# Performance work log

Measured on AMD Instinct MI355X. Metric: run time of the kernel, lower is better.

Reference implementation:

```python
import jax, jax.numpy as jnp
import numpy as np

N = 8192  # number of nodes


def _deg_norm(idx, n):
    # degree^{-1/2}, zero-degree clamped to 1 (DGL allow_zero_in_degree behavior)
    deg = jax.ops.segment_sum(jnp.ones(idx.shape[0], jnp.float32), idx, num_segments=n)
    return jax.lax.rsqrt(jnp.maximum(deg, 1.0))


def _graph_conv(h, src, dst, norm_src, norm_dst, W, b):
    # norm='both': scale at src, sparse sum-aggregate, scale at dst, then linear
    h = h * norm_src[:, None]
    m = jax.ops.segment_sum(h[src], dst, num_segments=h.shape[0])  # gather + scatter-add
    m = m * norm_dst[:, None]
    return m @ W + b


def setup_inputs() -> dict:
    key = jax.random.key(0)
    k = jax.random.split(key, 6)
    E = 262144
    x = jax.random.normal(k[0], (N, 256), jnp.float32)
    src = jax.random.randint(k[1], (E,), 0, N, jnp.int32)
    dst = jax.random.randint(k[2], (E,), 0, N, jnp.int32)
    W1 = jax.random.normal(k[3], (256, 128), jnp.float32) * (1.0 / np.sqrt(256))
    b1 = jnp.zeros((128,), jnp.float32)
    W2 = jax.random.normal(k[4], (128, 128), jnp.float32) * (1.0 / np.sqrt(128))
    b2 = jnp.zeros((128,), jnp.float32)
    return {"x": x, "src": src, "dst": dst, "W1": W1, "b1": b1, "W2": W2, "b2": b2}


def reference(x, src, dst, W1, b1, W2, b2):
    n = x.shape[0]
    norm_src = _deg_norm(src, n)  # out-degree norm
    norm_dst = _deg_norm(dst, n)  # in-degree norm
    # encode: GraphConv -> relu -> GraphConv  (dropout=0 -> identity)
    h = jax.nn.relu(_graph_conv(x, src, dst, norm_src, norm_dst, W1, b1))
    h = _graph_conv(h, src, dst, norm_src, norm_dst, W2, b2)
    # decode: sigmoid(h h^T), dense [N, N] reconstruction
    return jax.nn.sigmoid(h @ h.T)
```

## Files before the change

kernel.cpp:

```cpp
#include <hip/hip_runtime.h>
#include <hip/hip_bf16.h>

typedef __attribute__((ext_vector_type(8))) short short8;
typedef __attribute__((ext_vector_type(4))) float f32x4;

#define NNODES 8192
#define FDIM 128

__global__ void k_zero(int* __restrict__ p, int n) {
    int i = blockIdx.x * blockDim.x + threadIdx.x;
    if (i < n) p[i] = 0;
}

__global__ void k_deg_int(const int* __restrict__ src, const int* __restrict__ dst,
                          int* __restrict__ cnt_s, int* __restrict__ cnt_d, int E) {
    int e = blockIdx.x * blockDim.x + threadIdx.x;
    if (e < E) {
        atomicAdd(&cnt_s[src[e]], 1);
        atomicAdd(&cnt_d[dst[e]], 1);
    }
}

__global__ __launch_bounds__(256) void k_scan_norms(const int* __restrict__ cnt_s,
                                                    const int* __restrict__ cnt_d,
                                                    float* __restrict__ norm_s,
                                                    int* __restrict__ row_start,
                                                    int* __restrict__ cursor, int n) {
    __shared__ int partial[256];
    __shared__ int offs[257];
    int t = threadIdx.x;
    int base = t * 32;
#pragma unroll
    for (int i = 0; i < 32; ++i)
        norm_s[base + i] = rsqrtf(fmaxf((float)cnt_s[base + i], 1.0f));
    int local[32];
    int s = 0;
#pragma unroll
    for (int i = 0; i < 32; ++i) { local[i] = s; s += cnt_d[base + i]; }
    partial[t] = s;
    __syncthreads();
    if (t == 0) {
        int acc = 0;
        for (int i = 0; i < 256; ++i) { offs[i] = acc; acc += partial[i]; }
        offs[256] = acc;
    }
    __syncthreads();
    int o = offs[t];
#pragma unroll
    for (int i = 0; i < 32; ++i) {
        int v = o + local[i];
        row_start[base + i] = v;
        cursor[base + i] = v;
    }
    if (t == 0) row_start[n] = offs[256];
}

__global__ void k_fill(const int* __restrict__ src, const int* __restrict__ dst,
                       int* __restrict__ cursor, int* __restrict__ csr_src, int E) {
    int e = blockIdx.x * blockDim.x + threadIdx.x;
    if (e < E) {
        int pos = atomicAdd(&cursor[dst[e]], 1);
        csr_src[pos] = src[e];
    }
}

template<int K>
__global__ __launch_bounds__(256) void k_linear(const float* __restrict__ X,
                                                const float* __restrict__ W,
                                                const float* __restrict__ norm,
                                                float* __restrict__ Y) {
    __shared__ float xs[16][K];
    int t = threadIdx.x;
    int row0 = blockIdx.x * 16;
    constexpr int K4 = K / 4;
    constexpr int NCH = 16 * K4 / 256;
#pragma unroll
    for (int i = 0; i < NCH; ++i) {
        int c = t + i * 256;
        int r = c / K4, k4 = c % K4;
        *(float4*)&xs[r][k4 * 4] = *(const float4*)(X + (size_t)(row0 + r) * K + k4 * 4);
    }
    __syncthreads();

    int lane = t & 31, g = t >> 5;
    int r0 = g * 2, r1 = g * 2 + 1;
    int c = lane * 4;
    f32x4 acc0 = {0.f, 0.f, 0.f, 0.f}, acc1 = {0.f, 0.f, 0.f, 0.f};
    for (int k = 0; k < K; k += 4) {
        f32x4 x0 = *(f32x4*)&xs[r0][k];
        f32x4 x1 = *(f32x4*)&xs[r1][k];
#pragma unroll
        for (int kk = 0; kk < 4; ++kk) {
            f32x4 w = *(const f32x4*)(W + (size_t)(k + kk) * FDIM + c);
            acc0 += w * x0[kk];
            acc1 += w * x1[kk];
        }
    }
    float n0 = norm[row0 + r0], n1 = norm[row0 + r1];
    *(f32x4*)(Y + (size_t)(row0 + r0) * FDIM + c) = acc0 * n0;
    *(f32x4*)(Y + (size_t)(row0 + r1) * FDIM + c) = acc1 * n1;
}

static __device__ inline unsigned short f2bf(float f) {
    union { float f; unsigned int u; } a; a.f = f;
    unsigned int u = a.u;
    unsigned int r = u + 0x7FFFu + ((u >> 16) & 1u);
    return (unsigned short)(r >> 16);
}

template<int MODE>
__global__ __launch_bounds__(256) void k_gather_agg(const float* __restrict__ Y,
                                                    const int* __restrict__ row_start,
                                                    const int* __restrict__ csr_src,
                                                    const float* __restrict__ bias,
                                                    void* __restrict__ outp) {
    int t = threadIdx.x;
    int node = blockIdx.x * 8 + (t >> 5);
    int c4 = (t & 31) << 2;
    int beg = row_start[node], end = row_start[node + 1];
    f32x4 acc0 = {0.f, 0.f, 0.f, 0.f}, acc1 = {0.f, 0.f, 0.f, 0.f};
    int e = beg;
    for (; e + 3 < end; e += 4) {
        int s0 = csr_src[e], s1 = csr_src[e + 1], s2 = csr_src[e + 2], s3 = csr_src[e + 3];
        f32x4 v0 = *(const f32x4*)(Y + ((size_t)s0 << 7) + c4);
        f32x4 v1 = *(const f32x4*)(Y + ((size_t)s1 << 7) + c4);
        f32x4 v2 = *(const f32x4*)(Y + ((size_t)s2 << 7) + c4);
        f32x4 v3 = *(const f32x4*)(Y + ((size_t)s3 << 7) + c4);
        acc0 += v0; acc1 += v1; acc0 += v2; acc1 += v3;
    }
    for (; e < end; ++e) {
        int s0 = csr_src[e];
        acc0 += *(const f32x4*)(Y + ((size_t)s0 << 7) + c4);
    }
    f32x4 acc = acc0 + acc1;
    float scale = rsqrtf(fmaxf((float)(end - beg), 1.0f));
    f32x4 b = *(const f32x4*)(bias + c4);
    f32x4 v = acc * scale + b;
    if (MODE == 0) {
#pragma unroll
        for (int i = 0; i < 4; ++i) v[i] = fmaxf(v[i], 0.f);
        *(f32x4*)((float*)outp + ((size_t)node << 7) + c4) = v;
    } else {
        ushort4 u;
        u.x = f2bf(v[0]); u.y = f2bf(v[1]); u.z = f2bf(v[2]); u.w = f2bf(v[3]);
        *(ushort4*)((unsigned short*)outp + ((size_t)node << 7) + c4) = u;
    }
}

__global__ __launch_bounds__(256) void k_decode(const __hip_bfloat16* __restrict__ H,
                                                float* __restrict__ C) {
    const int ti = blockIdx.x, tj = blockIdx.y;
    if (tj < ti) return;
    __shared__ __align__(16) unsigned char smem[65536];
    unsigned char* sA = smem;
    unsigned char* sB = smem + 32768;
    const int t = threadIdx.x;
    const unsigned char* gH = (const unsigned char*)H;

#pragma unroll
    for (int i = 0; i < 8; ++i) {
        int chunk = t + i * 256;
        int row = chunk >> 4;
        int cc = (chunk & 15) << 4;
        int lofs = row * 256 + (cc ^ ((row & 7) << 4));
        *(float4*)(sA + lofs) = *(const float4*)(gH + ((size_t)(ti * 128 + row) << 8) + cc);
        *(float4*)(sB + lofs) = *(const float4*)(gH + ((size_t)(tj * 128 + row) << 8) + cc);
    }
    __syncthreads();

    const int w = t >> 6, lane = t & 63;
    const int wr = (w >> 1) * 64, wc = (w & 1) * 64;
    const int lr = lane & 15;
    const int lk = (lane >> 4) * 16;

    f32x4 acc[4][4] = {};

#pragma unroll
    for (int ks = 0; ks < 4; ++ks) {
        short8 af[4], bfr[4];
#pragma unroll
        for (int mi = 0; mi < 4; ++mi) {
            int row = wr + mi * 16 + lr;
            int off = row * 256 + ((ks * 64 + lk) ^ ((row & 7) << 4));
            af[mi] = *(const short8*)(sA + off);
        }
#pragma unroll
        for (int ni = 0; ni < 4; ++ni) {
            int row = wc + ni * 16 + lr;
            int off = row * 256 + ((ks * 64 + lk) ^ ((row & 7) << 4));
            bfr[ni] = *(const short8*)(sB + off);
        }
#pragma unroll
        for (int mi = 0; mi < 4; ++mi)
#pragma unroll
            for (int ni = 0; ni < 4; ++ni)
                acc[mi][ni] = __builtin_amdgcn_mfma_f32_16x16x32_bf16(af[mi], bfr[ni],
                                                                      acc[mi][ni], 0, 0, 0);
    }

    const int rbase = (lane >> 4) * 4;
    const int cbase = lane & 15;
#pragma unroll
    for (int mi = 0; mi < 4; ++mi) {
        int rowb = ti * 128 + wr + mi * 16 + rbase;
#pragma unroll
        for (int ni = 0; ni < 4; ++ni) {
            int col = tj * 128 + wc + ni * 16 + cbase;
            f32x4 s;
#pragma unroll
            for (int r = 0; r < 4; ++r)
                s[r] = 1.0f / (1.0f + __expf(-acc[mi][ni][r]));
            __builtin_nontemporal_store(s, (f32x4*)(C + (size_t)col * NNODES + rowb));
            if (ti != tj) {
#pragma unroll
                for (int r = 0; r < 4; ++r)
                    __builtin_nontemporal_store(s[r], C + (size_t)(rowb + r) * NNODES + col);
            }
        }
    }
}

extern "C" void kernel_launch(void* const* d_in, const int* in_sizes, int n_in,
                              void* d_out, int out_size, void* d_ws, size_t ws_size,
                              hipStream_t stream) {
    const float* x  = (const float*)d_in[0];
    const int* src  = (const int*)d_in[1];
    const int* dst  = (const int*)d_in[2];
    const float* W1 = (const float*)d_in[3];
    const float* b1 = (const float*)d_in[4];
    const float* W2 = (const float*)d_in[5];
    const float* b2 = (const float*)d_in[6];
    float* out = (float*)d_out;
    const int E = in_sizes[1];

    char* ws = (char*)d_ws;
    float* norm_s    = (float*)(ws + 0);
    int*   cnt_s     = (int*)(ws + (64 << 10));
    int*   cnt_d     = (int*)(ws + (96 << 10));
    int*   row_start = (int*)(ws + (128 << 10));
    int*   cursor    = (int*)(ws + (164 << 10));
    int*   csr_src   = (int*)(ws + (196 << 10));
    char*  big       = ws + (196 << 10) + ((size_t)E * 4);
    float* bufA      = (float*)big;
    float* bufB      = (float*)(big + (4 << 20));
    __hip_bfloat16* h2bf = (__hip_bfloat16*)(big + (8 << 20));

    k_zero<<<(2 * NNODES + 255) / 256, 256, 0, stream>>>(cnt_s, 2 * NNODES);

    k_deg_int<<<(E + 255) / 256, 256, 0, stream>>>(src, dst, cnt_s, cnt_d, E);
    k_scan_norms<<<1, 256, 0, stream>>>(cnt_s, cnt_d, norm_s, row_start, cursor, NNODES);
    k_fill<<<(E + 255) / 256, 256, 0, stream>>>(src, dst, cursor, csr_src, E);

    k_linear<256><<<NNODES / 16, 256, 0, stream>>>(x, W1, norm_s, bufA);
    k_gather_agg<0><<<NNODES / 8, 256, 0, stream>>>(bufA, row_start, csr_src, b1, bufB);

    k_linear<128><<<NNODES / 16, 256, 0, stream>>>(bufB, W2, norm_s, bufA);
    k_gather_agg<1><<<NNODES / 8, 256, 0, stream>>>(bufA, row_start, csr_src, b2, h2bf);

    k_decode<<<dim3(64, 64), 256, 0, stream>>>(h2bf, out);
}
```

Baseline: 211.9 us.

## Fuse encoder into cooperative persistent kernel and drop decode symmetry trick

Merges the degree count, scan, CSR fill, two linear layers and two gathers into one cooperative kernel with grid-wide syncs, keeping multi-kernel launches only as a fallback. This removes per-kernel launch gaps in the encoder but restricts it to 256 blocks. The decode kernel now computes every tile of the full N×N output instead of only the upper triangle with mirrored writes, and uses a fast reciprocal with plain row-major stores. That doubles the MFMA work in exchange for fully coalesced stores in place of strided transposed ones.

```diff
diff --git a/kernel.cpp b/kernel.cpp
--- a/kernel.cpp
+++ b/kernel.cpp
@@ -1,11 +1,168 @@
 #include <hip/hip_runtime.h>
 #include <hip/hip_bf16.h>
+#include <hip/hip_cooperative_groups.h>
+
+namespace cg = cooperative_groups;
 
 typedef __attribute__((ext_vector_type(8))) short short8;
 typedef __attribute__((ext_vector_type(4))) float f32x4;
 
 #define NNODES 8192
 #define FDIM 128
+
+static __device__ inline unsigned short f2bf(float f) {
+    union { float f; unsigned int u; } a; a.f = f;
+    unsigned int u = a.u;
+    unsigned int r = u + 0x7FFFu + ((u >> 16) & 1u);
+    return (unsigned short)(r >> 16);
+}
+
+template<int K>
+__device__ void lin_phase(const float* __restrict__ X, const float* __restrict__ W,
+                          const float* __restrict__ norm, float* __restrict__ Y,
+                          float* xs) {
+    const int t = threadIdx.x;
+    constexpr int K4 = K / 4;
+    constexpr int NCH = 16 * K4 / 256;
+    for (int tile = blockIdx.x; tile < NNODES / 16; tile += gridDim.x) {
+        int row0 = tile * 16;
+        __syncthreads();
+#pragma unroll
+        for (int i = 0; i < NCH; ++i) {
+            int c = t + i * 256;
+            int r = c / K4, k4 = c % K4;
+            *(float4*)&xs[r * K + k4 * 4] = *(const float4*)(X + (size_t)(row0 + r) * K + k4 * 4);
+        }
+        __syncthreads();
+        int lane = t & 31, g = t >> 5;
+        int r0 = g * 2, r1 = r0 + 1;
+        int c = lane * 4;
+        f32x4 acc0 = {0.f, 0.f, 0.f, 0.f}, acc1 = {0.f, 0.f, 0.f, 0.f};
+        for (int k = 0; k < K; k += 4) {
+            f32x4 x0 = *(f32x4*)&xs[r0 * K + k];
+            f32x4 x1 = *(f32x4*)&xs[r1 * K + k];
+#pragma unroll
+            for (int kk = 0; kk < 4; ++kk) {
+                f32x4 w = *(const f32x4*)(W + (size_t)(k + kk) * FDIM + c);
+                acc0 += w * x0[kk];
+                acc1 += w * x1[kk];
+            }
+        }
+        float n0 = norm[row0 + r0], n1 = norm[row0 + r1];
+        *(f32x4*)(Y + (size_t)(row0 + r0) * FDIM + c) = acc0 * n0;
+        *(f32x4*)(Y + (size_t)(row0 + r1) * FDIM + c) = acc1 * n1;
+    }
+}
+
+template<int MODE>
+__device__ void gather_phase(const float* __restrict__ Y, const int* __restrict__ row_start,
+                             const int* __restrict__ csr_src, const float* __restrict__ bias,
+                             void* __restrict__ outp) {
+    const int t = threadIdx.x;
+    const int c4 = (t & 31) << 2;
+    for (int node0 = blockIdx.x * 8; node0 < NNODES; node0 += gridDim.x * 8) {
+        int node = node0 + (t >> 5);
+        int beg = row_start[node], end = row_start[node + 1];
+        f32x4 acc0 = {0.f, 0.f, 0.f, 0.f}, acc1 = {0.f, 0.f, 0.f, 0.f};
+        int e = beg;
+        for (; e + 3 < end; e += 4) {
+            int s0 = csr_src[e], s1 = csr_src[e + 1], s2 = csr_src[e + 2], s3 = csr_src[e + 3];
+            f32x4 v0 = *(const f32x4*)(Y + ((size_t)s0 << 7) + c4);
+            f32x4 v1 = *(const f32x4*)(Y + ((size_t)s1 << 7) + c4);
+            f32x4 v2 = *(const f32x4*)(Y + ((size_t)s2 << 7) + c4);
+            f32x4 v3 = *(const f32x4*)(Y + ((size_t)s3 << 7) + c4);
+            acc0 += v0; acc1 += v1; acc0 += v2; acc1 += v3;
+        }
+        for (; e < end; ++e) {
+            int s0 = csr_src[e];
+            acc0 += *(const f32x4*)(Y + ((size_t)s0 << 7) + c4);
+        }
+        f32x4 acc = acc0 + acc1;
+        float scale = rsqrtf(fmaxf((float)(end - beg), 1.0f));
+        f32x4 b = *(const f32x4*)(bias + c4);
+        f32x4 v = acc * scale + b;
+        if (MODE == 0) {
+#pragma unroll
+            for (int i = 0; i < 4; ++i) v[i] = fmaxf(v[i], 0.f);
+            *(f32x4*)((float*)outp + ((size_t)node << 7) + c4) = v;
+        } else {
+            ushort4 u;
+            u.x = f2bf(v[0]); u.y = f2bf(v[1]); u.z = f2bf(v[2]); u.w = f2bf(v[3]);
+            *(ushort4*)((unsigned short*)outp + ((size_t)node << 7) + c4) = u;
+        }
+    }
+}
+
+struct EncArgs {
+    const int* src; const int* dst; int E;
+    int* cnt;
+    float* norm_s; int* row_start; int* cursor; int* csr_src;
+    const float* x; const float* W1; const float* b1;
+    const float* W2; const float* b2;
+    float* bufA; float* bufB; unsigned short* h2;
+};
+
+__global__ __launch_bounds__(256) void k_encode(EncArgs a) {
+    cg::grid_group grid = cg::this_grid();
+    __shared__ __align__(16) float xs[16 * 256];
+    const int t = threadIdx.x;
+    const int gid = blockIdx.x * 256 + t;
+    const int gsz = gridDim.x * 256;
+
+    for (int i = gid; i < 2 * NNODES; i += gsz) a.cnt[i] = 0;
+    grid.sync();
+
+    for (int e = gid; e < a.E; e += gsz) {
+        atomicAdd(&a.cnt[a.src[e]], 1);
+        atomicAdd(&a.cnt[NNODES + a.dst[e]], 1);
+    }
+    grid.sync();
+
+    for (int i = gid; i < NNODES; i += gsz)
+        a.norm_s[i] = rsqrtf(fmaxf((float)a.cnt[i], 1.0f));
+    if (blockIdx.x == 0) {
+        int* partial = (int*)xs;
+        int* offs = partial + 256;
+        const int* cnt_d = a.cnt + NNODES;
+        int base = t * 32;
+        int local[32];
+        int s = 0;
+#pragma unroll
+        for (int i = 0; i < 32; ++i) { local[i] = s; s += cnt_d[base + i]; }
+        partial[t] = s;
+        __syncthreads();
+        if (t == 0) {
+            int acc = 0;
+            for (int i = 0; i < 256; ++i) { offs[i] = acc; acc += partial[i]; }
+            offs[256] = acc;
+        }
+        __syncthreads();
+        int o = offs[t];
+#pragma unroll
+        for (int i = 0; i < 32; ++i) {
+            int v = o + local[i];
+            a.row_start[base + i] = v;
+            a.cursor[base + i] = v;
+        }
+        if (t == 0) a.row_start[NNODES] = offs[256];
+    }
+    grid.sync();
+
+    for (int e = gid; e < a.E; e += gsz) {
+        int pos = atomicAdd(&a.cursor[a.dst[e]], 1);
+        a.csr_src[pos] = a.src[e];
+    }
+    lin_phase<256>(a.x, a.W1, a.norm_s, a.bufA, xs);
+    grid.sync();
+
+    gather_phase<0>(a.bufA, a.row_start, a.csr_src, a.b1, a.bufB);
+    grid.sync();
+
+    lin_phase<128>(a.bufB, a.W2, a.norm_s, a.bufA, xs);
+    grid.sync();
+
+    gather_phase<1>(a.bufA, a.row_start, a.csr_src, a.b2, a.h2);
+}
 
 __global__ void k_zero(int* __restrict__ p, int n) {
     int i = blockIdx.x * blockDim.x + threadIdx.x;
@@ -13,16 +170,15 @@
 }
 
 __global__ void k_deg_int(const int* __restrict__ src, const int* __restrict__ dst,
-                          int* __restrict__ cnt_s, int* __restrict__ cnt_d, int E) {
+                          int* __restrict__ cnt, int E) {
     int e = blockIdx.x * blockDim.x + threadIdx.x;
     if (e < E) {
-        atomicAdd(&cnt_s[src[e]], 1);
-        atomicAdd(&cnt_d[dst[e]], 1);
-    }
-}
-
-__global__ __launch_bounds__(256) void k_scan_norms(const int* __restrict__ cnt_s,
-                                                    const int* __restrict__ cnt_d,
+        atomicAdd(&cnt[src[e]], 1);
+        atomicAdd(&cnt[NNODES + dst[e]], 1);
+    }
+}
+
+__global__ __launch_bounds__(256) void k_scan_norms(const int* __restrict__ cnt,
                                                     float* __restrict__ norm_s,
                                                     int* __restrict__ row_start,
                                                     int* __restrict__ cursor, int n) {
@@ -30,9 +186,10 @@
     __shared__ int offs[257];
     int t = threadIdx.x;
     int base = t * 32;
+    const int* cnt_d = cnt + NNODES;
 #pragma unroll
     for (int i = 0; i < 32; ++i)
-        norm_s[base + i] = rsqrtf(fmaxf((float)cnt_s[base + i], 1.0f));
+        norm_s[base + i] = rsqrtf(fmaxf((float)cnt[base + i], 1.0f));
     int local[32];
     int s = 0;
 #pragma unroll
@@ -65,95 +222,29 @@
 }
 
 template<int K>
-__global__ __launch_bounds__(256) void k_linear(const float* __restrict__ X,
-                                                const float* __restrict__ W,
-                                                const float* __restrict__ norm,
-                                                float* __restrict__ Y) {
-    __shared__ float xs[16][K];
-    int t = threadIdx.x;
-    int row0 = blockIdx.x * 16;
-    constexpr int K4 = K / 4;
-    constexpr int NCH = 16 * K4 / 256;
-#pragma unroll
-    for (int i = 0; i < NCH; ++i) {
-        int c = t + i * 256;
-        int r = c / K4, k4 = c % K4;
-        *(float4*)&xs[r][k4 * 4] = *(const float4*)(X + (size_t)(row0 + r) * K + k4 * 4);
-    }
-    __syncthreads();
-
-    int lane = t & 31, g = t >> 5;
-    int r0 = g * 2, r1 = g * 2 + 1;
-    int c = lane * 4;
-    f32x4 acc0 = {0.f, 0.f, 0.f, 0.f}, acc1 = {0.f, 0.f, 0.f, 0.f};
-    for (int k = 0; k < K; k += 4) {
-        f32x4 x0 = *(f32x4*)&xs[r0][k];
-        f32x4 x1 = *(f32x4*)&xs[r1][k];
-#pragma unroll
-        for (int kk = 0; kk < 4; ++kk) {
-            f32x4 w = *(const f32x4*)(W + (size_t)(k + kk) * FDIM + c);
-            acc0 += w * x0[kk];
-            acc1 += w * x1[kk];
-        }
-    }
-    float n0 = norm[row0 + r0], n1 = norm[row0 + r1];
-    *(f32x4*)(Y + (size_t)(row0 + r0) * FDIM + c) = acc0 * n0;
-    *(f32x4*)(Y + (size_t)(row0 + r1) * FDIM + c) = acc1 * n1;
-}
-
-static __device__ inline unsigned short f2bf(float f) {
-    union { float f; unsigned int u; } a; a.f = f;
-    unsigned int u = a.u;
-    unsigned int r = u + 0x7FFFu + ((u >> 16) & 1u);
-    return (unsigned short)(r >> 16);
+__global__ __launch_bounds__(256) void k_lin(const float* __restrict__ X,
+                                             const float* __restrict__ W,
+                                             const float* __restrict__ norm,
+                                             float* __restrict__ Y) {
+    __shared__ __align__(16) float xs[16 * K];
+    lin_phase<K>(X, W, norm, Y, xs);
 }
 
 template<int MODE>
-__global__ __launch_bounds__(256) void k_gather_agg(const float* __restrict__ Y,
-                                                    const int* __restrict__ row_start,
-                                                    const int* __restrict__ csr_src,
-                                                    const float* __restrict__ bias,
-                                                    void* __restrict__ outp) {
-    int t = threadIdx.x;
-    int node = blockIdx.x * 8 + (t >> 5);
-    int c4 = (t & 31) << 2;
-    int beg = row_start[node], end = row_start[node + 1];
-    f32x4 acc0 = {0.f, 0.f, 0.f, 0.f}, acc1 = {0.f, 0.f, 0.f, 0.f};
-    int e = beg;
-    for (; e + 3 < end; e += 4) {
-        int s0 = csr_src[e], s1 = csr_src[e + 1], s2 = csr_src[e + 2], s3 = csr_src[e + 3];
-        f32x4 v0 = *(const f32x4*)(Y + ((size_t)s0 << 7) + c4);
-        f32x4 v1 = *(const f32x4*)(Y + ((size_t)s1 << 7) + c4);
-        f32x4 v2 = *(const f32x4*)(Y + ((size_t)s2 << 7) + c4);
-        f32x4 v3 = *(const f32x4*)(Y + ((size_t)s3 << 7) + c4);
-        acc0 += v0; acc1 += v1; acc0 += v2; acc1 += v3;
-    }
-    for (; e < end; ++e) {
-        int s0 = csr_src[e];
-        acc0 += *(const f32x4*)(Y + ((size_t)s0 << 7) + c4);
-    }
-    f32x4 acc = acc0 + acc1;
-    float scale = rsqrtf(fmaxf((float)(end - beg), 1.0f));
-    f32x4 b = *(const f32x4*)(bias + c4);
-    f32x4 v = acc * scale + b;
-    if (MODE == 0) {
-#pragma unroll
-        for (int i = 0; i < 4; ++i) v[i] = fmaxf(v[i], 0.f);
-        *(f32x4*)((float*)outp + ((size_t)node << 7) + c4) = v;
-    } else {
-        ushort4 u;
-        u.x = f2bf(v[0]); u.y = f2bf(v[1]); u.z = f2bf(v[2]); u.w = f2bf(v[3]);
-        *(ushort4*)((unsigned short*)outp + ((size_t)node << 7) + c4) = u;
-    }
+__global__ __launch_bounds__(256) void k_gat(const float* __restrict__ Y,
+                                             const int* __restrict__ row_start,
+                                             const int* __restrict__ csr_src,
+                                             const float* __restrict__ bias,
+                                             void* __restrict__ outp) {
+    gather_phase<MODE>(Y, row_start, csr_src, bias, outp);
 }
 
 __global__ __launch_bounds__(256) void k_decode(const __hip_bfloat16* __restrict__ H,
                                                 float* __restrict__ C) {
-    const int ti = blockIdx.x, tj = blockIdx.y;
-    if (tj < ti) return;
     __shared__ __align__(16) unsigned char smem[65536];
     unsigned char* sA = smem;
     unsigned char* sB = smem + 32768;
+    const int ti = blockIdx.x, tj = blockIdx.y;
     const int t = threadIdx.x;
     const unsigned char* gH = (const unsigned char*)H;
 
@@ -206,15 +297,10 @@
 #pragma unroll
         for (int ni = 0; ni < 4; ++ni) {
             int col = tj * 128 + wc + ni * 16 + cbase;
-            f32x4 s;
-#pragma unroll
-            for (int r = 0; r < 4; ++r)
-                s[r] = 1.0f / (1.0f + __expf(-acc[mi][ni][r]));
-            __builtin_nontemporal_store(s, (f32x4*)(C + (size_t)col * NNODES + rowb));
-            if (ti != tj) {
-#pragma unroll
-                for (int r = 0; r < 4; ++r)
-                    __builtin_nontemporal_store(s[r], C + (size_t)(rowb + r) * NNODES + col);
+#pragma unroll
+            for (int r = 0; r < 4; ++r) {
+                float s = __builtin_amdgcn_rcpf(1.0f + __expf(-acc[mi][ni][r]));
+                C[(size_t)(rowb + r) * NNODES + col] = s;
             }
         }
     }
@@ -235,27 +321,36 @@
 
     char* ws = (char*)d_ws;
     float* norm_s    = (float*)(ws + 0);
-    int*   cnt_s     = (int*)(ws + (64 << 10));
-    int*   cnt_d     = (int*)(ws + (96 << 10));
-    int*   row_start = (int*)(ws + (128 << 10));
-    int*   cursor    = (int*)(ws + (164 << 10));
-    int*   csr_src   = (int*)(ws + (196 << 10));
-    char*  big       = ws + (196 << 10) + ((size_t)E * 4);
+    int*   cnt       = (int*)(ws + (32 << 10));
+    int*   row_start = (int*)(ws + (96 << 10));
+    int*   cursor    = (int*)(ws + (132 << 10));
+    int*   csr_src   = (int*)(ws + (164 << 10));
+    char*  big       = ws + (164 << 10) + ((size_t)E * 4);
     float* bufA      = (float*)big;
     float* bufB      = (float*)(big + (4 << 20));
     __hip_bfloat16* h2bf = (__hip_bfloat16*)(big + (8 << 20));
 
-    k_zero<<<(2 * NNODES + 255) / 256, 256, 0, stream>>>(cnt_s, 2 * NNODES);
-
-    k_deg_int<<<(E + 255) / 256, 256, 0, stream>>>(src, dst, cnt_s, cnt_d, E);
-    k_scan_norms<<<1, 256, 0, stream>>>(cnt_s, cnt_d, norm_s, row_start, cursor, NNODES);
-    k_fill<<<(E + 255) / 256, 256, 0, stream>>>(src, dst, cursor, csr_src, E);
-
-    k_linear<256><<<NNODES / 16, 256, 0, stream>>>(x, W1, norm_s, bufA);
-    k_gather_agg<0><<<NNODES / 8, 256, 0, stream>>>(bufA, row_start, csr_src, b1, bufB);
-
-    k_linear<128><<<NNODES / 16, 256, 0, stream>>>(bufB, W2, norm_s, bufA);
-    k_gather_agg<1><<<NNODES / 8, 256, 0, stream>>>(bufA, row_start, csr_src, b2, h2bf);
+    EncArgs ea;
+    ea.src = src; ea.dst = dst; ea.E = E;
+    ea.cnt = cnt; ea.norm_s = norm_s; ea.row_start = row_start;
+    ea.cursor = cursor; ea.csr_src = csr_src;
+    ea.x = x; ea.W1 = W1; ea.b1 = b1; ea.W2 = W2; ea.b2 = b2;
+    ea.bufA = bufA; ea.bufB = bufB; ea.h2 = (unsigned short*)h2bf;
+
+    void* kp[] = { &ea };
+    hipError_t cerr = hipLaunchCooperativeKernel((const void*)k_encode, dim3(256), dim3(256),
+                                                 kp, 0, stream);
+    if (cerr != hipSuccess) {
+        (void)hipGetLastError();
+        k_zero<<<(2 * NNODES + 255) / 256, 256, 0, stream>>>(cnt, 2 * NNODES);
+        k_deg_int<<<(E + 255) / 256, 256, 0, stream>>>(src, dst, cnt, E);
+        k_scan_norms<<<1, 256, 0, stream>>>(cnt, norm_s, row_start, cursor, NNODES);
+        k_fill<<<(E + 255) / 256, 256, 0, stream>>>(src, dst, cursor, csr_src, E);
+        k_lin<256><<<NNODES / 16, 256, 0, stream>>>(x, W1, norm_s, bufA);
+        k_gat<0><<<NNODES / 8, 256, 0, stream>>>(bufA, row_start, csr_src, b1, bufB);
+        k_lin<128><<<NNODES / 16, 256, 0, stream>>>(bufB, W2, norm_s, bufA);
+        k_gat<1><<<NNODES / 8, 256, 0, stream>>>(bufA, row_start, csr_src, b2, h2bf);
+    }
 
     k_decode<<<dim3(64, 64), 256, 0, stream>>>(h2bf, out);
 }
```

Result: slower. 392.0 us (+85.0%).

## Fuse second linear into first aggregation and compute full decode grid

Applied to the files above, without the earlier changes.

The first gather-aggregate now runs the W2 projection itself from shared memory, which removes one kernel launch and an 8192x128 intermediate round trip. The decoder no longer exploits symmetry: every block computes its own tile and writes it row-major with normal stores, where before only upper-triangle tiles ran and each wrote both the tile and its transpose. This doubles the MFMA work in exchange for coalesced, non-transposed writes. It also merges the degree counters into one array, shrinks the zeroing launch and uses a hardware reciprocal for the sigmoid.

```diff
diff --git a/kernel.cpp b/kernel.cpp
--- a/kernel.cpp
+++ b/kernel.cpp
@@ -6,6 +6,13 @@
 
 #define NNODES 8192
 #define FDIM 128
+
+static __device__ inline unsigned short f2bf(float f) {
+    union { float f; unsigned int u; } a; a.f = f;
+    unsigned int u = a.u;
+    unsigned int r = u + 0x7FFFu + ((u >> 16) & 1u);
+    return (unsigned short)(r >> 16);
+}
 
 __global__ void k_zero(int* __restrict__ p, int n) {
     int i = blockIdx.x * blockDim.x + threadIdx.x;
@@ -13,16 +20,15 @@
 }
 
 __global__ void k_deg_int(const int* __restrict__ src, const int* __restrict__ dst,
-                          int* __restrict__ cnt_s, int* __restrict__ cnt_d, int E) {
+                          int* __restrict__ cnt, int E) {
     int e = blockIdx.x * blockDim.x + threadIdx.x;
     if (e < E) {
-        atomicAdd(&cnt_s[src[e]], 1);
-        atomicAdd(&cnt_d[dst[e]], 1);
-    }
-}
-
-__global__ __launch_bounds__(256) void k_scan_norms(const int* __restrict__ cnt_s,
-                                                    const int* __restrict__ cnt_d,
+        atomicAdd(&cnt[src[e]], 1);
+        atomicAdd(&cnt[NNODES + dst[e]], 1);
+    }
+}
+
+__global__ __launch_bounds__(256) void k_scan_norms(const int* __restrict__ cnt,
                                                     float* __restrict__ norm_s,
                                                     int* __restrict__ row_start,
                                                     int* __restrict__ cursor, int n) {
@@ -30,9 +36,10 @@
     __shared__ int offs[257];
     int t = threadIdx.x;
     int base = t * 32;
+    const int* cnt_d = cnt + NNODES;
 #pragma unroll
     for (int i = 0; i < 32; ++i)
-        norm_s[base + i] = rsqrtf(fmaxf((float)cnt_s[base + i], 1.0f));
+        norm_s[base + i] = rsqrtf(fmaxf((float)cnt[base + i], 1.0f));
     int local[32];
     int s = 0;
 #pragma unroll
@@ -65,10 +72,10 @@
 }
 
 template<int K>
-__global__ __launch_bounds__(256) void k_linear(const float* __restrict__ X,
-                                                const float* __restrict__ W,
-                                                const float* __restrict__ norm,
-                                                float* __restrict__ Y) {
+__global__ __launch_bounds__(256) void k_lin(const float* __restrict__ X,
+                                             const float* __restrict__ W,
+                                             const float* __restrict__ norm,
+                                             float* __restrict__ Y) {
     __shared__ float xs[16][K];
     int t = threadIdx.x;
     int row0 = blockIdx.x * 16;
@@ -83,7 +90,7 @@
     __syncthreads();
 
     int lane = t & 31, g = t >> 5;
-    int r0 = g * 2, r1 = g * 2 + 1;
+    int r0 = g * 2, r1 = r0 + 1;
     int c = lane * 4;
     f32x4 acc0 = {0.f, 0.f, 0.f, 0.f}, acc1 = {0.f, 0.f, 0.f, 0.f};
     for (int k = 0; k < K; k += 4) {
@@ -101,19 +108,61 @@
     *(f32x4*)(Y + (size_t)(row0 + r1) * FDIM + c) = acc1 * n1;
 }
 
-static __device__ inline unsigned short f2bf(float f) {
-    union { float f; unsigned int u; } a; a.f = f;
-    unsigned int u = a.u;
-    unsigned int r = u + 0x7FFFu + ((u >> 16) & 1u);
-    return (unsigned short)(r >> 16);
-}
-
-template<int MODE>
-__global__ __launch_bounds__(256) void k_gather_agg(const float* __restrict__ Y,
-                                                    const int* __restrict__ row_start,
-                                                    const int* __restrict__ csr_src,
-                                                    const float* __restrict__ bias,
-                                                    void* __restrict__ outp) {
+__global__ __launch_bounds__(256) void k_gatlin(const float* __restrict__ Y,
+                                                const int* __restrict__ row_start,
+                                                const int* __restrict__ csr_src,
+                                                const float* __restrict__ b1,
+                                                const float* __restrict__ W2,
+                                                const float* __restrict__ norm_s,
+                                                float* __restrict__ Y2) {
+    __shared__ float h1s[8][132];
+    const int t = threadIdx.x;
+    const int g = t >> 5, lane = t & 31;
+    const int node = blockIdx.x * 8 + g;
+    const int c4 = lane << 2;
+
+    int beg = row_start[node], end = row_start[node + 1];
+    f32x4 acc0 = {0.f, 0.f, 0.f, 0.f}, acc1 = {0.f, 0.f, 0.f, 0.f};
+    int e = beg;
+    for (; e + 3 < end; e += 4) {
+        int s0 = csr_src[e], s1 = csr_src[e + 1], s2 = csr_src[e + 2], s3 = csr_src[e + 3];
+        f32x4 v0 = *(const f32x4*)(Y + ((size_t)s0 << 7) + c4);
+        f32x4 v1 = *(const f32x4*)(Y + ((size_t)s1 << 7) + c4);
+        f32x4 v2 = *(const f32x4*)(Y + ((size_t)s2 << 7) + c4);
+        f32x4 v3 = *(const f32x4*)(Y + ((size_t)s3 << 7) + c4);
+        acc0 += v0; acc1 += v1; acc0 += v2; acc1 += v3;
+    }
+    for (; e < end; ++e) {
+        int s0 = csr_src[e];
+        acc0 += *(const f32x4*)(Y + ((size_t)s0 << 7) + c4);
+    }
+    f32x4 acc = acc0 + acc1;
+    float scale = rsqrtf(fmaxf((float)(end - beg), 1.0f));
+    f32x4 b = *(const f32x4*)(b1 + c4);
+    f32x4 v = acc * scale + b;
+#pragma unroll
+    for (int i = 0; i < 4; ++i) v[i] = fmaxf(v[i], 0.f);
+    *(f32x4*)&h1s[g][c4] = v;
+    __syncthreads();
+
+    f32x4 acc2 = {0.f, 0.f, 0.f, 0.f};
+    for (int k = 0; k < FDIM; k += 4) {
+        f32x4 xv = *(f32x4*)&h1s[g][k];
+#pragma unroll
+        for (int kk = 0; kk < 4; ++kk) {
+            f32x4 w = *(const f32x4*)(W2 + (size_t)(k + kk) * FDIM + c4);
+            acc2 += w * xv[kk];
+        }
+    }
+    float ns = norm_s[node];
+    *(f32x4*)(Y2 + ((size_t)node << 7) + c4) = acc2 * ns;
+}
+
+__global__ __launch_bounds__(256) void k_gat2(const float* __restrict__ Y,
+                                              const int* __restrict__ row_start,
+                                              const int* __restrict__ csr_src,
+                                              const float* __restrict__ bias,
+                                              unsigned short* __restrict__ outp) {
     int t = threadIdx.x;
     int node = blockIdx.x * 8 + (t >> 5);
     int c4 = (t & 31) << 2;
@@ -136,24 +185,17 @@
     float scale = rsqrtf(fmaxf((float)(end - beg), 1.0f));
     f32x4 b = *(const f32x4*)(bias + c4);
     f32x4 v = acc * scale + b;
-    if (MODE == 0) {
-#pragma unroll
-        for (int i = 0; i < 4; ++i) v[i] = fmaxf(v[i], 0.f);
-        *(f32x4*)((float*)outp + ((size_t)node << 7) + c4) = v;
-    } else {
-        ushort4 u;
-        u.x = f2bf(v[0]); u.y = f2bf(v[1]); u.z = f2bf(v[2]); u.w = f2bf(v[3]);
-        *(ushort4*)((unsigned short*)outp + ((size_t)node << 7) + c4) = u;
-    }
+    ushort4 u;
+    u.x = f2bf(v[0]); u.y = f2bf(v[1]); u.z = f2bf(v[2]); u.w = f2bf(v[3]);
+    *(ushort4*)(outp + ((size_t)node << 7) + c4) = u;
 }
 
 __global__ __launch_bounds__(256) void k_decode(const __hip_bfloat16* __restrict__ H,
                                                 float* __restrict__ C) {
-    const int ti = blockIdx.x, tj = blockIdx.y;
-    if (tj < ti) return;
     __shared__ __align__(16) unsigned char smem[65536];
     unsigned char* sA = smem;
     unsigned char* sB = smem + 32768;
+    const int ti = blockIdx.x, tj = blockIdx.y;
     const int t = threadIdx.x;
     const unsigned char* gH = (const unsigned char*)H;
 
@@ -206,15 +248,10 @@
 #pragma unroll
         for (int ni = 0; ni < 4; ++ni) {
             int col = tj * 128 + wc + ni * 16 + cbase;
-            f32x4 s;
-#pragma unroll
-            for (int r = 0; r < 4; ++r)
-                s[r] = 1.0f / (1.0f + __expf(-acc[mi][ni][r]));
-            __builtin_nontemporal_store(s, (f32x4*)(C + (size_t)col * NNODES + rowb));
-            if (ti != tj) {
-#pragma unroll
-                for (int r = 0; r < 4; ++r)
-                    __builtin_nontemporal_store(s[r], C + (size_t)(rowb + r) * NNODES + col);
+#pragma unroll
+            for (int r = 0; r < 4; ++r) {
+                float s = __builtin_amdgcn_rcpf(1.0f + __expf(-acc[mi][ni][r]));
+                C[(size_t)(rowb + r) * NNODES + col] = s;
             }
         }
     }
@@ -235,27 +272,24 @@
 
     char* ws = (char*)d_ws;
     float* norm_s    = (float*)(ws + 0);
-    int*   cnt_s     = (int*)(ws + (64 << 10));
-    int*   cnt_d     = (int*)(ws + (96 << 10));
-    int*   row_start = (int*)(ws + (128 << 10));
-    int*   cursor    = (int*)(ws + (164 << 10));
-    int*   csr_src   = (int*)(ws + (196 << 10));
-    char*  big       = ws + (196 << 10) + ((size_t)E * 4);
+    int*   cnt       = (int*)(ws + (32 << 10));
+    int*   row_start = (int*)(ws + (96 << 10));
+    int*   cursor    = (int*)(ws + (132 << 10));
+    int*   csr_src   = (int*)(ws + (164 << 10));
+    char*  big       = ws + (164 << 10) + ((size_t)E * 4);
     float* bufA      = (float*)big;
     float* bufB      = (float*)(big + (4 << 20));
     __hip_bfloat16* h2bf = (__hip_bfloat16*)(big + (8 << 20));
 
-    k_zero<<<(2 * NNODES + 255) / 256, 256, 0, stream>>>(cnt_s, 2 * NNODES);
-
-    k_deg_int<<<(E + 255) / 256, 256, 0, stream>>>(src, dst, cnt_s, cnt_d, E);
-    k_scan_norms<<<1, 256, 0, stream>>>(cnt_s, cnt_d, norm_s, row_start, cursor, NNODES);
+    k_zero<<<64, 256, 0, stream>>>(cnt, 2 * NNODES);
+
+    k_deg_int<<<(E + 255) / 256, 256, 0, stream>>>(src, dst, cnt, E);
+    k_scan_norms<<<1, 256, 0, stream>>>(cnt, norm_s, row_start, cursor, NNODES);
     k_fill<<<(E + 255) / 256, 256, 0, stream>>>(src, dst, cursor, csr_src, E);
 
-    k_linear<256><<<NNODES / 16, 256, 0, stream>>>(x, W1, norm_s, bufA);
-    k_gather_agg<0><<<NNODES / 8, 256, 0, stream>>>(bufA, row_start, csr_src, b1, bufB);
-
-    k_linear<128><<<NNODES / 16, 256, 0, stream>>>(bufB, W2, norm_s, bufA);
-    k_gather_agg<1><<<NNODES / 8, 256, 0, stream>>>(bufA, row_start, csr_src, b2, h2bf);
+    k_lin<256><<<NNODES / 16, 256, 0, stream>>>(x, W1, norm_s, bufA);
+    k_gatlin<<<NNODES / 8, 256, 0, stream>>>(bufA, row_start, csr_src, b1, W2, norm_s, bufB);
+    k_gat2<<<NNODES / 8, 256, 0, stream>>>(bufB, row_start, csr_src, b2, (unsigned short*)h2bf);
 
     k_decode<<<dim3(64, 64), 256, 0, stream>>>(h2bf, out);
 }
```

Result: faster. 177.5 us (-16.2%).
